# Kernel optimization log

Measured on AMD Instinct MI355X. Metric: run time of the kernel, lower is better.

Reference implementation:

```python
import jax, jax.numpy as jnp
import numpy as np
import math

SIZE = 64
NLAND = 8
N_ITER = 6


def setup_inputs() -> dict:
    key = jax.random.key(0)
    k1, k2, k3 = jax.random.split(key, 3)
    B, T, C = 4, 4096, 1024
    return {
        "q": jax.random.normal(k1, (B, T, C), dtype=jnp.float32),
        "k": jax.random.normal(k2, (B, T, C), dtype=jnp.float32),
        "v": jax.random.normal(k3, (B, T, C), dtype=jnp.float32),
    }


def _iterative_pinv(mat, n_iter=N_ITER):
    # Newton-Schulz iteration for pseudo-inverse of [..., m, m] kernel.
    m = mat.shape[-1]
    I = jnp.eye(m, dtype=mat.dtype)
    K = mat
    # NOTE: torch.max over the whole tensor (global scalar), faithful to source.
    V = (1.0 / jnp.max(jnp.sum(K, axis=-2))) * jnp.swapaxes(K, -1, -2)
    for _ in range(n_iter):
        KV = jnp.matmul(K, V)
        V = jnp.matmul(0.25 * V, 13.0 * I - jnp.matmul(KV, 15.0 * I - jnp.matmul(KV, 7.0 * I - KV)))
    return V


def reference(q, k, v):
    B, T, C = q.shape
    H = C // SIZE
    scale = 1.0 / math.sqrt(SIZE)
    # Faithful reshape (not transpose) as in the source module.
    qh = q.reshape(B, H, T, SIZE)
    kh = k.reshape(B, H, T, SIZE)
    vh = v.reshape(B, H, T, SIZE)
    # T % NLAND == 0 branch: landmark = segment mean over T//NLAND tokens.
    q_l = qh.reshape(B, H, NLAND, T // NLAND, SIZE).mean(axis=-2)  # [B,H,m,d]
    k_l = kh.reshape(B, H, NLAND, T // NLAND, SIZE).mean(axis=-2)
    kernel_1 = jax.nn.softmax(jnp.einsum('bhtd,bhmd->bhtm', qh, k_l) * scale, axis=-1)  # [B,H,T,m]
    kernel_2 = jax.nn.softmax(jnp.einsum('bhmd,bhnd->bhmn', q_l, k_l) * scale, axis=-1)  # [B,H,m,m]
    kernel_3 = jax.nn.softmax(jnp.einsum('bhmd,bhtd->bhmt', q_l, kh) * scale, axis=-1)  # [B,H,m,T]
    pinv = _iterative_pinv(kernel_2)  # [B,H,m,m]
    k3v = jnp.matmul(kernel_3, vh)    # [B,H,m,d]
    out = jnp.matmul(jnp.matmul(kernel_1, pinv), k3v)  # [B,H,T,d]
    return out.reshape(B, T, C)
```

## Files before the change

### kernel.cpp

```cpp
#include <hip/hip_runtime.h>
#include <math.h>

#define T_TOK 4096
#define DD 64
#define NHEADS 64
#define SEG 512
#define NCHUNK 32
#define CHUNK 128
#define TILE 32
#define SCALE 0.125f

#define QL_OFF   0
#define KL_OFF   32768
#define K2_OFF   65536
#define CS_OFF   69632
#define PINV_OFF 70144
#define LPQ_OFF  74240
#define KP_OFF   205312
#define PA_OFF   336384
#define PD_OFF   1384960
#define W2_OFF   1401344

__global__ __launch_bounds__(256) void qsum_kernel(
    const float* __restrict__ q, float* __restrict__ ws) {
  int tid = threadIdx.x;
  const float4* q4 = (const float4*)q + (size_t)blockIdx.x * 2048;
  float4 a = make_float4(0.f, 0.f, 0.f, 0.f);
#pragma unroll
  for (int it = 0; it < 8; ++it) {
    float4 x = q4[it * 256 + tid];
    a.x += x.x; a.y += x.y; a.z += x.z; a.w += x.w;
  }
  __shared__ float4 red[16][17];
  red[tid >> 4][tid & 15] = a;
  __syncthreads();
  if (tid < 16) {
    float4 s = make_float4(0.f, 0.f, 0.f, 0.f);
#pragma unroll
    for (int g = 0; g < 16; ++g) {
      float4 r = red[g][tid];
      s.x += r.x; s.y += r.y; s.z += r.z; s.w += r.w;
    }
    ((float4*)(ws + LPQ_OFF))[blockIdx.x * 16 + tid] = s;
  }
}

__global__ __launch_bounds__(512) void prepq_kernel(float* __restrict__ ws) {
  int hb = blockIdx.x, tid = threadIdx.x;
  int m = tid >> 6, d = tid & 63;
  float s = 0.f;
#pragma unroll
  for (int c2 = 0; c2 < 4; ++c2)
    s += ws[LPQ_OFF + (size_t)(hb * 32 + m * 4 + c2) * 64 + d];
  ws[QL_OFF + hb * 512 + tid] = s * (1.f / (float)SEG);
}

__global__ __launch_bounds__(256) void k3v_kernel(
    const float* __restrict__ k, const float* __restrict__ v,
    float* __restrict__ ws) {
  int hb = blockIdx.x >> 5, c = blockIdx.x & 31;
  int tid = threadIdx.x;
  int w = tid >> 6, lane = tid & 63;
  __shared__ float ql[8][68];
  __shared__ float kt[TILE][68];
  __shared__ float vt[TILE][68];
  __shared__ float pl[TILE][9];
  __shared__ float denp[4][8];

  if (tid < 128) {
    float4 x = ((const float4*)(ws + QL_OFF))[hb * 128 + tid];
    *(float4*)&ql[tid >> 4][(tid & 15) * 4] = x;
  }
  size_t base4 = ((size_t)hb * T_TOK + (size_t)c * CHUNK) * 16;
  float a0 = 0.f, a1 = 0.f, dden = 0.f, ksum = 0.f;

  for (int tile = 0; tile < 4; ++tile) {
    __syncthreads();
    const float4* k4 = (const float4*)k + base4 + tile * TILE * 16;
    const float4* v4 = (const float4*)v + base4 + tile * TILE * 16;
    {
      float4 x0 = k4[tid], x1 = k4[tid + 256];
      float4 y0 = v4[tid], y1 = v4[tid + 256];
      *(float4*)&kt[tid >> 4][(tid & 15) * 4] = x0;
      *(float4*)&kt[(tid + 256) >> 4][(tid & 15) * 4] = x1;
      *(float4*)&vt[tid >> 4][(tid & 15) * 4] = y0;
      *(float4*)&vt[(tid + 256) >> 4][(tid & 15) * 4] = y1;
    }
    __syncthreads();
    {
      int t = tid >> 3, m = tid & 7;
      const float4* kr = (const float4*)&kt[t][0];
      const float4* qr = (const float4*)&ql[m][0];
      float dot = 0.f;
#pragma unroll
      for (int d4 = 0; d4 < 16; ++d4) {
        float4 kk = kr[d4], qq = qr[d4];
        dot += kk.x * qq.x + kk.y * qq.y + kk.z * qq.z + kk.w * qq.w;
      }
      float p = __expf(dot * SCALE);
      pl[t][m] = p;
      float r = p;
      r += __shfl_xor(r, 8);
      r += __shfl_xor(r, 16);
      r += __shfl_xor(r, 32);
      if (lane < 8) denp[w][lane] = r;
    }
    __syncthreads();
    {
#pragma unroll
      for (int t = 0; t < TILE; ++t) {
        float vv = vt[t][lane];
        a0 += pl[t][w] * vv;
        a1 += pl[t][w + 4] * vv;
      }
      if (w == 0) {
#pragma unroll
        for (int t = 0; t < TILE; ++t) ksum += kt[t][lane];
      }
      if (tid < 8)
        dden += denp[0][tid] + denp[1][tid] + denp[2][tid] + denp[3][tid];
    }
  }
  ws[PA_OFF + (((size_t)hb * NCHUNK + c) * 8 + w) * 64 + lane] = a0;
  ws[PA_OFF + (((size_t)hb * NCHUNK + c) * 8 + w + 4) * 64 + lane] = a1;
  if (tid < 8) ws[PD_OFF + (hb * NCHUNK + c) * 8 + tid] = dden;
  if (tid < 64) ws[KP_OFF + (size_t)(hb * NCHUNK + c) * 64 + tid] = ksum;
}

__global__ __launch_bounds__(512) void prepk_kernel(float* __restrict__ ws) {
  int hb = blockIdx.x, tid = threadIdx.x;
  __shared__ float qls[8][68];
  __shared__ float kls[8][68];
  __shared__ float ee[8][9];
  int m = tid >> 6, d = tid & 63;
  float s = 0.f;
#pragma unroll
  for (int c2 = 0; c2 < 4; ++c2)
    s += ws[KP_OFF + (size_t)(hb * 32 + m * 4 + c2) * 64 + d];
  s *= (1.f / (float)SEG);
  kls[m][d] = s;
  ws[KL_OFF + hb * 512 + tid] = s;
  qls[m][d] = ws[QL_OFF + hb * 512 + tid];
  __syncthreads();
  if (tid < 64) {
    int i = tid >> 3, j = tid & 7;
    float dot = 0.f;
#pragma unroll
    for (int dd = 0; dd < 64; ++dd) dot += qls[i][dd] * kls[j][dd];
    ee[i][j] = __expf(dot * SCALE);
  }
  __syncthreads();
  if (tid < 64) {
    int i = tid >> 3, j = tid & 7;
    float ssum = 0.f;
#pragma unroll
    for (int jj = 0; jj < 8; ++jj) ssum += ee[i][jj];
    ws[K2_OFF + hb * 64 + tid] = ee[i][j] / ssum;
  }
  if (tid < 8) {
    float cs = 0.f;
    for (int ii = 0; ii < 8; ++ii) {
      float ssum = 0.f;
#pragma unroll
      for (int jj = 0; jj < 8; ++jj) ssum += ee[ii][jj];
      cs += ee[ii][tid] / ssum;
    }
    ws[CS_OFF + hb * 8 + tid] = cs;
  }
}

__global__ __launch_bounds__(64) void pinv_kernel(float* __restrict__ ws) {
  int hb = blockIdx.x;
  int tid = threadIdx.x;
  float mx = 0.f;
  for (int t = 0; t < 8; ++t) mx = fmaxf(mx, ws[CS_OFF + t * 64 + tid]);
  for (int off = 32; off; off >>= 1) mx = fmaxf(mx, __shfl_xor(mx, off));
  float inv = 1.f / mx;

  int i = tid >> 3, j = tid & 7;
  __shared__ float K[8][9], V[8][9], X[8][9], Y[8][9];
  K[i][j] = ws[K2_OFF + hb * 64 + tid];
  V[i][j] = ws[K2_OFF + hb * 64 + j * 8 + i] * inv;
  __syncthreads();
  for (int it = 0; it < 6; ++it) {
    float x = 0.f;
    for (int kk = 0; kk < 8; ++kk) x += K[i][kk] * V[kk][j];
    X[i][j] = x;
    __syncthreads();
    float bm = 0.f;
    for (int kk = 0; kk < 8; ++kk) bm += X[i][kk] * X[kk][j];
    bm = 7.f * x - bm;
    Y[i][j] = bm;
    __syncthreads();
    float dm = 0.f;
    for (int kk = 0; kk < 8; ++kk) dm += X[i][kk] * Y[kk][j];
    dm = 15.f * x - dm;
    __syncthreads();
    Y[i][j] = dm;
    __syncthreads();
    float vd = 0.f;
    for (int kk = 0; kk < 8; ++kk) vd += V[i][kk] * Y[kk][j];
    float vn = 0.25f * (13.f * V[i][j] - vd);
    __syncthreads();
    V[i][j] = vn;
    __syncthreads();
  }
  ws[PINV_OFF + hb * 64 + tid] = V[i][j];
}

__global__ __launch_bounds__(512) void redw2_kernel(float* __restrict__ ws) {
  int hb = blockIdx.x, tid = threadIdx.x;
  __shared__ float k3vs[8][68];
  __shared__ float pv[8][9];
  int m = tid >> 6, d = tid & 63;
  float s = 0.f, den = 0.f;
  for (int c = 0; c < NCHUNK; ++c) {
    s += ws[PA_OFF + (((size_t)hb * NCHUNK + c) * 8 + m) * 64 + d];
    den += ws[PD_OFF + (hb * NCHUNK + c) * 8 + m];
  }
  k3vs[m][d] = s / den;
  if (tid < 64) pv[tid >> 3][tid & 7] = ws[PINV_OFF + hb * 64 + tid];
  __syncthreads();
  float o = 0.f;
#pragma unroll
  for (int j = 0; j < 8; ++j) o += pv[m][j] * k3vs[j][d];
  ws[W2_OFF + hb * 512 + tid] = o;
}

__global__ __launch_bounds__(256) void out_kernel(
    const float* __restrict__ q, float* __restrict__ out,
    const float* __restrict__ ws) {
  int hb = blockIdx.x >> 6, tt = blockIdx.x & 63;
  int tid = threadIdx.x;
  __shared__ float qt[64][68];
  __shared__ float klh[8][68];
  __shared__ float w2s[8][68];
  __shared__ float pl[64][9];

  if (tid < 128) {
    float4 x = ((const float4*)(ws + KL_OFF))[hb * 128 + tid];
    *(float4*)&klh[tid >> 4][(tid & 15) * 4] = x;
    float4 y = ((const float4*)(ws + W2_OFF))[hb * 128 + tid];
    *(float4*)&w2s[tid >> 4][(tid & 15) * 4] = y;
  }
  size_t base4 = ((size_t)hb * T_TOK + (size_t)tt * 64) * 16;
  const float4* q4 = (const float4*)q + base4;
#pragma unroll
  for (int it = 0; it < 4; ++it) {
    int f4 = it * 256 + tid;
    float4 x = q4[f4];
    *(float4*)&qt[f4 >> 4][(f4 & 15) * 4] = x;
  }
  __syncthreads();
#pragma unroll
  for (int p = 0; p < 2; ++p) {
    int idx = p * 256 + tid;
    int t = idx >> 3, m = idx & 7;
    const float4* qr = (const float4*)&qt[t][0];
    const float4* kr = (const float4*)&klh[m][0];
    float dot = 0.f;
#pragma unroll
    for (int d4 = 0; d4 < 16; ++d4) {
      float4 a = qr[d4], b = kr[d4];
      dot += a.x * b.x + a.y * b.y + a.z * b.z + a.w * b.w;
    }
    pl[t][m] = __expf(dot * SCALE);
  }
  __syncthreads();
  float4* o4 = (float4*)out + base4;
#pragma unroll
  for (int i = 0; i < 4; ++i) {
    int t = i * 16 + (tid >> 4);
    int qd = tid & 15;
    float p0 = pl[t][0], p1 = pl[t][1], p2 = pl[t][2], p3 = pl[t][3];
    float p4 = pl[t][4], p5 = pl[t][5], p6 = pl[t][6], p7 = pl[t][7];
    float inv = 1.f / (p0 + p1 + p2 + p3 + p4 + p5 + p6 + p7);
    float4 acc = make_float4(0.f, 0.f, 0.f, 0.f);
    float pm[8] = {p0, p1, p2, p3, p4, p5, p6, p7};
#pragma unroll
    for (int m2 = 0; m2 < 8; ++m2) {
      float w = pm[m2] * inv;
      float4 wv = *(const float4*)&w2s[m2][qd * 4];
      acc.x += w * wv.x; acc.y += w * wv.y; acc.z += w * wv.z; acc.w += w * wv.w;
    }
    o4[i * 256 + tid] = acc;
  }
}

extern "C" void kernel_launch(void* const* d_in, const int* in_sizes, int n_in,
                              void* d_out, int out_size, void* d_ws, size_t ws_size,
                              hipStream_t stream) {
  const float* q = (const float*)d_in[0];
  const float* k = (const float*)d_in[1];
  const float* v = (const float*)d_in[2];
  float* out = (float*)d_out;
  float* ws = (float*)d_ws;

  qsum_kernel<<<2048, 256, 0, stream>>>(q, ws);
  prepq_kernel<<<NHEADS, 512, 0, stream>>>(ws);
  k3v_kernel<<<NHEADS * NCHUNK, 256, 0, stream>>>(k, v, ws);
  prepk_kernel<<<NHEADS, 512, 0, stream>>>(ws);
  pinv_kernel<<<NHEADS, 64, 0, stream>>>(ws);
  redw2_kernel<<<NHEADS, 512, 0, stream>>>(ws);
  out_kernel<<<NHEADS * 64, 256, 0, stream>>>(q, out, ws);
}
```

Baseline: 93.05 us.

## Fuse q/k landmark sums, move k sums out of k3v, use register-resident dot products

```diff
diff --git a/kernel.cpp b/kernel.cpp
--- a/kernel.cpp
+++ b/kernel.cpp
@@ -7,7 +7,6 @@
 #define SEG 512
 #define NCHUNK 32
 #define CHUNK 128
-#define TILE 32
 #define SCALE 0.125f
 
 #define QL_OFF   0
@@ -16,131 +15,61 @@
 #define CS_OFF   69632
 #define PINV_OFF 70144
 #define LPQ_OFF  74240
-#define KP_OFF   205312
-#define PA_OFF   336384
-#define PD_OFF   1384960
-#define W2_OFF   1401344
-
-__global__ __launch_bounds__(256) void qsum_kernel(
-    const float* __restrict__ q, float* __restrict__ ws) {
-  int tid = threadIdx.x;
-  const float4* q4 = (const float4*)q + (size_t)blockIdx.x * 2048;
-  float4 a = make_float4(0.f, 0.f, 0.f, 0.f);
+#define LPK_OFF  598528
+#define PA_OFF   74240
+#define PD_OFF   1122816
+#define W2_OFF   1139200
+
+__global__ __launch_bounds__(256) void sum12_kernel(
+    const float* __restrict__ q, const float* __restrict__ k,
+    float* __restrict__ ws) {
+  int tid = threadIdx.x;
+  int w = tid >> 6, lane = tid & 63;
+  size_t base4 = (size_t)blockIdx.x * 2048 + (size_t)w * 512;
+  const float4* q4 = (const float4*)q + base4;
+  const float4* k4 = (const float4*)k + base4;
+  float4 aq = make_float4(0.f, 0.f, 0.f, 0.f);
+  float4 ak = make_float4(0.f, 0.f, 0.f, 0.f);
 #pragma unroll
   for (int it = 0; it < 8; ++it) {
-    float4 x = q4[it * 256 + tid];
-    a.x += x.x; a.y += x.y; a.z += x.z; a.w += x.w;
-  }
-  __shared__ float4 red[16][17];
-  red[tid >> 4][tid & 15] = a;
-  __syncthreads();
-  if (tid < 16) {
-    float4 s = make_float4(0.f, 0.f, 0.f, 0.f);
-#pragma unroll
-    for (int g = 0; g < 16; ++g) {
-      float4 r = red[g][tid];
-      s.x += r.x; s.y += r.y; s.z += r.z; s.w += r.w;
-    }
-    ((float4*)(ws + LPQ_OFF))[blockIdx.x * 16 + tid] = s;
-  }
-}
-
-__global__ __launch_bounds__(512) void prepq_kernel(float* __restrict__ ws) {
-  int hb = blockIdx.x, tid = threadIdx.x;
-  int m = tid >> 6, d = tid & 63;
-  float s = 0.f;
-#pragma unroll
-  for (int c2 = 0; c2 < 4; ++c2)
-    s += ws[LPQ_OFF + (size_t)(hb * 32 + m * 4 + c2) * 64 + d];
-  ws[QL_OFF + hb * 512 + tid] = s * (1.f / (float)SEG);
-}
-
-__global__ __launch_bounds__(256) void k3v_kernel(
-    const float* __restrict__ k, const float* __restrict__ v,
-    float* __restrict__ ws) {
-  int hb = blockIdx.x >> 5, c = blockIdx.x & 31;
-  int tid = threadIdx.x;
-  int w = tid >> 6, lane = tid & 63;
-  __shared__ float ql[8][68];
-  __shared__ float kt[TILE][68];
-  __shared__ float vt[TILE][68];
-  __shared__ float pl[TILE][9];
-  __shared__ float denp[4][8];
-
-  if (tid < 128) {
-    float4 x = ((const float4*)(ws + QL_OFF))[hb * 128 + tid];
-    *(float4*)&ql[tid >> 4][(tid & 15) * 4] = x;
-  }
-  size_t base4 = ((size_t)hb * T_TOK + (size_t)c * CHUNK) * 16;
-  float a0 = 0.f, a1 = 0.f, dden = 0.f, ksum = 0.f;
-
-  for (int tile = 0; tile < 4; ++tile) {
-    __syncthreads();
-    const float4* k4 = (const float4*)k + base4 + tile * TILE * 16;
-    const float4* v4 = (const float4*)v + base4 + tile * TILE * 16;
-    {
-      float4 x0 = k4[tid], x1 = k4[tid + 256];
-      float4 y0 = v4[tid], y1 = v4[tid + 256];
-      *(float4*)&kt[tid >> 4][(tid & 15) * 4] = x0;
-      *(float4*)&kt[(tid + 256) >> 4][(tid & 15) * 4] = x1;
-      *(float4*)&vt[tid >> 4][(tid & 15) * 4] = y0;
-      *(float4*)&vt[(tid + 256) >> 4][(tid & 15) * 4] = y1;
-    }
-    __syncthreads();
-    {
-      int t = tid >> 3, m = tid & 7;
-      const float4* kr = (const float4*)&kt[t][0];
-      const float4* qr = (const float4*)&ql[m][0];
-      float dot = 0.f;
-#pragma unroll
-      for (int d4 = 0; d4 < 16; ++d4) {
-        float4 kk = kr[d4], qq = qr[d4];
-        dot += kk.x * qq.x + kk.y * qq.y + kk.z * qq.z + kk.w * qq.w;
-      }
-      float p = __expf(dot * SCALE);
-      pl[t][m] = p;
-      float r = p;
-      r += __shfl_xor(r, 8);
-      r += __shfl_xor(r, 16);
-      r += __shfl_xor(r, 32);
-      if (lane < 8) denp[w][lane] = r;
-    }
-    __syncthreads();
-    {
-#pragma unroll
-      for (int t = 0; t < TILE; ++t) {
-        float vv = vt[t][lane];
-        a0 += pl[t][w] * vv;
-        a1 += pl[t][w + 4] * vv;
-      }
-      if (w == 0) {
-#pragma unroll
-        for (int t = 0; t < TILE; ++t) ksum += kt[t][lane];
-      }
-      if (tid < 8)
-        dden += denp[0][tid] + denp[1][tid] + denp[2][tid] + denp[3][tid];
-    }
-  }
-  ws[PA_OFF + (((size_t)hb * NCHUNK + c) * 8 + w) * 64 + lane] = a0;
-  ws[PA_OFF + (((size_t)hb * NCHUNK + c) * 8 + w + 4) * 64 + lane] = a1;
-  if (tid < 8) ws[PD_OFF + (hb * NCHUNK + c) * 8 + tid] = dden;
-  if (tid < 64) ws[KP_OFF + (size_t)(hb * NCHUNK + c) * 64 + tid] = ksum;
-}
-
-__global__ __launch_bounds__(512) void prepk_kernel(float* __restrict__ ws) {
+    float4 x = q4[it * 64 + lane];
+    aq.x += x.x; aq.y += x.y; aq.z += x.z; aq.w += x.w;
+    float4 y = k4[it * 64 + lane];
+    ak.x += y.x; ak.y += y.y; ak.z += y.z; ak.w += y.w;
+  }
+#pragma unroll
+  for (int s = 16; s <= 32; s <<= 1) {
+    aq.x += __shfl_xor(aq.x, s, 64); aq.y += __shfl_xor(aq.y, s, 64);
+    aq.z += __shfl_xor(aq.z, s, 64); aq.w += __shfl_xor(aq.w, s, 64);
+    ak.x += __shfl_xor(ak.x, s, 64); ak.y += __shfl_xor(ak.y, s, 64);
+    ak.z += __shfl_xor(ak.z, s, 64); ak.w += __shfl_xor(ak.w, s, 64);
+  }
+  if (lane < 16) {
+    size_t gw = (size_t)blockIdx.x * 4 + w;
+    ((float4*)(ws + LPQ_OFF))[gw * 16 + lane] = aq;
+    ((float4*)(ws + LPK_OFF))[gw * 16 + lane] = ak;
+  }
+}
+
+__global__ __launch_bounds__(512) void prep_kernel(float* __restrict__ ws) {
   int hb = blockIdx.x, tid = threadIdx.x;
   __shared__ float qls[8][68];
   __shared__ float kls[8][68];
   __shared__ float ee[8][9];
   int m = tid >> 6, d = tid & 63;
-  float s = 0.f;
-#pragma unroll
-  for (int c2 = 0; c2 < 4; ++c2)
-    s += ws[KP_OFF + (size_t)(hb * 32 + m * 4 + c2) * 64 + d];
-  s *= (1.f / (float)SEG);
-  kls[m][d] = s;
-  ws[KL_OFF + hb * 512 + tid] = s;
-  qls[m][d] = ws[QL_OFF + hb * 512 + tid];
+  float sq = 0.f, sk = 0.f;
+#pragma unroll
+  for (int c = 0; c < 16; ++c) {
+    size_t idx = (size_t)(hb * 128 + m * 16 + c) * 64 + d;
+    sq += ws[LPQ_OFF + idx];
+    sk += ws[LPK_OFF + idx];
+  }
+  sq *= (1.f / (float)SEG);
+  sk *= (1.f / (float)SEG);
+  qls[m][d] = sq;
+  kls[m][d] = sk;
+  ws[QL_OFF + hb * 512 + tid] = sq;
+  ws[KL_OFF + hb * 512 + tid] = sk;
   __syncthreads();
   if (tid < 64) {
     int i = tid >> 3, j = tid & 7;
@@ -174,7 +103,7 @@
   int tid = threadIdx.x;
   float mx = 0.f;
   for (int t = 0; t < 8; ++t) mx = fmaxf(mx, ws[CS_OFF + t * 64 + tid]);
-  for (int off = 32; off; off >>= 1) mx = fmaxf(mx, __shfl_xor(mx, off));
+  for (int off = 32; off; off >>= 1) mx = fmaxf(mx, __shfl_xor(mx, off, 64));
   float inv = 1.f / mx;
 
   int i = tid >> 3, j = tid & 7;
@@ -206,6 +135,85 @@
     __syncthreads();
   }
   ws[PINV_OFF + hb * 64 + tid] = V[i][j];
+}
+
+__global__ __launch_bounds__(256) void k3v_kernel(
+    const float* __restrict__ k, const float* __restrict__ v,
+    float* __restrict__ ws) {
+  int tid = threadIdx.x;
+  int w = tid >> 6, lane = tid & 63, q4i = lane & 15;
+  int hb = blockIdx.x >> 5, c = blockIdx.x & 31;
+
+  float4 qlf[8];
+#pragma unroll
+  for (int m = 0; m < 8; ++m)
+    qlf[m] = ((const float4*)(ws + QL_OFF))[hb * 128 + m * 16 + q4i];
+
+  size_t base4 = ((size_t)hb * T_TOK + (size_t)c * CHUNK + (size_t)w * 32) * 16;
+  const float4* k4 = (const float4*)k + base4;
+  const float4* v4 = (const float4*)v + base4;
+
+  float4 acc[8];
+  float den[8];
+#pragma unroll
+  for (int m = 0; m < 8; ++m) {
+    acc[m] = make_float4(0.f, 0.f, 0.f, 0.f);
+    den[m] = 0.f;
+  }
+
+#pragma unroll 2
+  for (int it = 0; it < 8; ++it) {
+    float4 kk = k4[it * 64 + lane];
+    float4 vv = v4[it * 64 + lane];
+    float p[8];
+#pragma unroll
+    for (int m = 0; m < 8; ++m) {
+      float dp = kk.x * qlf[m].x + kk.y * qlf[m].y + kk.z * qlf[m].z + kk.w * qlf[m].w;
+      dp += __shfl_xor(dp, 1, 64);
+      dp += __shfl_xor(dp, 2, 64);
+      dp += __shfl_xor(dp, 4, 64);
+      dp += __shfl_xor(dp, 8, 64);
+      p[m] = __expf(dp * SCALE);
+    }
+#pragma unroll
+    for (int m = 0; m < 8; ++m) {
+      acc[m].x += p[m] * vv.x; acc[m].y += p[m] * vv.y;
+      acc[m].z += p[m] * vv.z; acc[m].w += p[m] * vv.w;
+      den[m] += p[m];
+    }
+  }
+#pragma unroll
+  for (int m = 0; m < 8; ++m) {
+#pragma unroll
+    for (int s = 16; s <= 32; s <<= 1) {
+      acc[m].x += __shfl_xor(acc[m].x, s, 64);
+      acc[m].y += __shfl_xor(acc[m].y, s, 64);
+      acc[m].z += __shfl_xor(acc[m].z, s, 64);
+      acc[m].w += __shfl_xor(acc[m].w, s, 64);
+      den[m] += __shfl_xor(den[m], s, 64);
+    }
+  }
+  __shared__ float4 accs[4][8][16];
+  __shared__ float dens[4][8];
+  if (lane < 16) {
+#pragma unroll
+    for (int m = 0; m < 8; ++m) accs[w][m][q4i] = acc[m];
+  }
+  if (lane == 0) {
+#pragma unroll
+    for (int m = 0; m < 8; ++m) dens[w][m] = den[m];
+  }
+  __syncthreads();
+  if (tid < 128) {
+    int m = tid >> 4, i = tid & 15;
+    float4 a = accs[0][m][i], b = accs[1][m][i], cc = accs[2][m][i], dd = accs[3][m][i];
+    float4 s = make_float4(a.x + b.x + cc.x + dd.x, a.y + b.y + cc.y + dd.y,
+                           a.z + b.z + cc.z + dd.z, a.w + b.w + cc.w + dd.w);
+    ((float4*)(ws + PA_OFF))[((size_t)(hb * 32 + c) * 8 + m) * 16 + i] = s;
+  }
+  if (tid < 8)
+    ws[PD_OFF + (hb * 32 + c) * 8 + tid] =
+        dens[0][tid] + dens[1][tid] + dens[2][tid] + dens[3][tid];
 }
 
 __global__ __launch_bounds__(512) void redw2_kernel(float* __restrict__ ws) {
@@ -230,60 +238,44 @@
 __global__ __launch_bounds__(256) void out_kernel(
     const float* __restrict__ q, float* __restrict__ out,
     const float* __restrict__ ws) {
-  int hb = blockIdx.x >> 6, tt = blockIdx.x & 63;
-  int tid = threadIdx.x;
-  __shared__ float qt[64][68];
-  __shared__ float klh[8][68];
-  __shared__ float w2s[8][68];
-  __shared__ float pl[64][9];
-
-  if (tid < 128) {
-    float4 x = ((const float4*)(ws + KL_OFF))[hb * 128 + tid];
-    *(float4*)&klh[tid >> 4][(tid & 15) * 4] = x;
-    float4 y = ((const float4*)(ws + W2_OFF))[hb * 128 + tid];
-    *(float4*)&w2s[tid >> 4][(tid & 15) * 4] = y;
-  }
-  size_t base4 = ((size_t)hb * T_TOK + (size_t)tt * 64) * 16;
+  int tid = threadIdx.x;
+  int w = tid >> 6, lane = tid & 63, q4i = lane & 15;
+  int hb = blockIdx.x >> 5, c = blockIdx.x & 31;
+
+  float4 klf[8], w2f[8];
+#pragma unroll
+  for (int m = 0; m < 8; ++m) {
+    klf[m] = ((const float4*)(ws + KL_OFF))[hb * 128 + m * 16 + q4i];
+    w2f[m] = ((const float4*)(ws + W2_OFF))[hb * 128 + m * 16 + q4i];
+  }
+  size_t base4 = ((size_t)hb * T_TOK + (size_t)c * CHUNK + (size_t)w * 32) * 16;
   const float4* q4 = (const float4*)q + base4;
-#pragma unroll
-  for (int it = 0; it < 4; ++it) {
-    int f4 = it * 256 + tid;
-    float4 x = q4[f4];
-    *(float4*)&qt[f4 >> 4][(f4 & 15) * 4] = x;
-  }
-  __syncthreads();
-#pragma unroll
-  for (int p = 0; p < 2; ++p) {
-    int idx = p * 256 + tid;
-    int t = idx >> 3, m = idx & 7;
-    const float4* qr = (const float4*)&qt[t][0];
-    const float4* kr = (const float4*)&klh[m][0];
-    float dot = 0.f;
-#pragma unroll
-    for (int d4 = 0; d4 < 16; ++d4) {
-      float4 a = qr[d4], b = kr[d4];
-      dot += a.x * b.x + a.y * b.y + a.z * b.z + a.w * b.w;
-    }
-    pl[t][m] = __expf(dot * SCALE);
-  }
-  __syncthreads();
   float4* o4 = (float4*)out + base4;
-#pragma unroll
-  for (int i = 0; i < 4; ++i) {
-    int t = i * 16 + (tid >> 4);
-    int qd = tid & 15;
-    float p0 = pl[t][0], p1 = pl[t][1], p2 = pl[t][2], p3 = pl[t][3];
-    float p4 = pl[t][4], p5 = pl[t][5], p6 = pl[t][6], p7 = pl[t][7];
-    float inv = 1.f / (p0 + p1 + p2 + p3 + p4 + p5 + p6 + p7);
-    float4 acc = make_float4(0.f, 0.f, 0.f, 0.f);
-    float pm[8] = {p0, p1, p2, p3, p4, p5, p6, p7};
-#pragma unroll
-    for (int m2 = 0; m2 < 8; ++m2) {
-      float w = pm[m2] * inv;
-      float4 wv = *(const float4*)&w2s[m2][qd * 4];
-      acc.x += w * wv.x; acc.y += w * wv.y; acc.z += w * wv.z; acc.w += w * wv.w;
-    }
-    o4[i * 256 + tid] = acc;
+
+#pragma unroll 2
+  for (int it = 0; it < 8; ++it) {
+    float4 qq = q4[it * 64 + lane];
+    float p[8];
+    float s = 0.f;
+#pragma unroll
+    for (int m = 0; m < 8; ++m) {
+      float dp = qq.x * klf[m].x + qq.y * klf[m].y + qq.z * klf[m].z + qq.w * klf[m].w;
+      dp += __shfl_xor(dp, 1, 64);
+      dp += __shfl_xor(dp, 2, 64);
+      dp += __shfl_xor(dp, 4, 64);
+      dp += __shfl_xor(dp, 8, 64);
+      p[m] = __expf(dp * SCALE);
+      s += p[m];
+    }
+    float inv = 1.f / s;
+    float4 o = make_float4(0.f, 0.f, 0.f, 0.f);
+#pragma unroll
+    for (int m = 0; m < 8; ++m) {
+      float wgt = p[m] * inv;
+      o.x += wgt * w2f[m].x; o.y += wgt * w2f[m].y;
+      o.z += wgt * w2f[m].z; o.w += wgt * w2f[m].w;
+    }
+    o4[it * 64 + lane] = o;
   }
 }
 
@@ -296,11 +288,10 @@
   float* out = (float*)d_out;
   float* ws = (float*)d_ws;
 
-  qsum_kernel<<<2048, 256, 0, stream>>>(q, ws);
-  prepq_kernel<<<NHEADS, 512, 0, stream>>>(ws);
+  sum12_kernel<<<2048, 256, 0, stream>>>(q, k, ws);
+  prep_kernel<<<NHEADS, 512, 0, stream>>>(ws);
+  pinv_kernel<<<NHEADS, 64, 0, stream>>>(ws);
   k3v_kernel<<<NHEADS * NCHUNK, 256, 0, stream>>>(k, v, ws);
-  prepk_kernel<<<NHEADS, 512, 0, stream>>>(ws);
-  pinv_kernel<<<NHEADS, 64, 0, stream>>>(ws);
   redw2_kernel<<<NHEADS, 512, 0, stream>>>(ws);
-  out_kernel<<<NHEADS * 64, 256, 0, stream>>>(q, out, ws);
-}
+  out_kernel<<<NHEADS * NCHUNK, 256, 0, stream>>>(q, out, ws);
+}
```

Result: slower. 109.2 us (+17.4%).
